# Optimization experiments

Measured on AMD Instinct MI355X. Metric: run time of the kernel, lower is better.

Reference implementation:

```python
import jax, jax.numpy as jnp
import numpy as np

B = 128          # batch of predictions
C = 1024         # number of constraints
N = 512          # number of atoms appearing in constraints (minimal subset)
NUM_CLASSES = 1024
BODY_P = 0.02    # body sparsity


def setup_inputs() -> dict:
    rng = np.random.default_rng(0)
    # distinct sorted atom indices into the full class space
    atoms = np.sort(rng.permutation(NUM_CLASSES)[:N]).astype(np.int64)
    # each constraint has one head literal: one-hot in pos_head OR neg_head
    head_atom = rng.integers(0, N, size=C)
    head_sign = rng.random(C) < 0.5
    pos_head = np.zeros((C, N), np.float32)
    neg_head = np.zeros((C, N), np.float32)
    rows = np.arange(C)
    pos_head[rows[head_sign], head_atom[head_sign]] = 1.0
    neg_head[rows[~head_sign], head_atom[~head_sign]] = 1.0
    # sparse disjoint 0/1 body masks, head atom excluded from its own body
    pos_body = (rng.random((C, N)) < BODY_P).astype(np.float32)
    neg_body = ((rng.random((C, N)) < BODY_P) & (pos_body == 0)).astype(np.float32)
    pos_body[rows, head_atom] = 0.0
    neg_body[rows, head_atom] = 0.0
    key = jax.random.key(0)
    preds = jax.random.uniform(key, (B, NUM_CLASSES), dtype=jnp.float32)  # probs in [0,1]
    return {
        "preds": preds,
        "pos_head": jnp.asarray(pos_head),
        "neg_head": jnp.asarray(neg_head),
        "pos_body": jnp.asarray(pos_body),
        "neg_body": jnp.asarray(neg_body),
        "atoms": jnp.asarray(atoms),
    }


def reference(preds, pos_head, neg_head, pos_body, neg_body, atoms):
    # to_minimal: gather atom subset  [B, N]
    m = preds[:, atoms]
    # body_rev[b,c,j] = pos_body + m*(neg_body - pos_body)
    #   = (1-m) where body literal positive, m where negative, 0 otherwise
    body_rev = pos_body[None] + m[:, None, :] * (neg_body - pos_body)[None]  # [B,C,N]
    # candidate body satisfaction degree per constraint
    body_min = 1.0 - jnp.max(body_rev, axis=2)  # [B,C]
    # scatter candidates to head atoms via one-hot head masks (max-reduce over cons)
    lb = jnp.max(body_min[:, :, None] * pos_head[None], axis=1)        # [B,N]
    ub = 1.0 - jnp.max(body_min[:, :, None] * neg_head[None], axis=1)  # [B,N]
    lo = jnp.minimum(lb, ub)
    hi = jnp.maximum(lb, ub)
    updated = jnp.maximum(lo, jnp.minimum(hi, m))
    # from_minimal: scatter updated atoms back into full prediction vector
    return preds.at[:, atoms].set(updated)
```

## Files before the change

### kernel.cpp

```cpp
#include <hip/hip_runtime.h>

#define Bsz 128
#define Csz 1024
#define Nsz 512
#define NCsz 1024
#define CAP 64

__global__ __launch_bounds__(256) void k_pre(
    const float* __restrict__ preds,
    const float* __restrict__ pos_head, const float* __restrict__ neg_head,
    const float* __restrict__ pos_body, const float* __restrict__ neg_body,
    const int* __restrict__ atoms,
    float* __restrict__ mT, unsigned* __restrict__ bounds,
    int* __restrict__ pos_list, int* __restrict__ neg_list,
    int* __restrict__ pos_cnt, int* __restrict__ neg_cnt,
    int* __restrict__ head_of,
    float* __restrict__ out)
{
    int blk = blockIdx.x, tid = threadIdx.x;
    if (blk < 128) {
        ((uint4*)bounds)[blk * 256 + tid] = make_uint4(0u, 0u, 0u, 0u);
    } else if (blk < 384) {
        int b   = tid & (Bsz - 1);
        int col = 2 * (blk - 128) + (tid >> 7);
        mT[col * Bsz + b] = preds[b * NCsz + atoms[col]];
    } else if (blk < 640) {
        __shared__ int cnts[4][2];
        int wave = tid >> 6, lane = tid & 63;
        int c = (blk - 384) * 4 + wave;
        if (lane == 0) { cnts[wave][0] = 0; cnts[wave][1] = 0; }
        const float4* pb4 = (const float4*)(pos_body + c * Nsz);
        const float4* nb4 = (const float4*)(neg_body + c * Nsz);
        const float4* ph4 = (const float4*)(pos_head + c * Nsz);
        const float4* nh4 = (const float4*)(neg_head + c * Nsz);
        for (int k = 0; k < 2; k++) {
            int q = k * 64 + lane;
            float4 p  = pb4[q];
            float4 nb = nb4[q];
            float4 ph = ph4[q];
            float4 nh = nh4[q];
            int n0 = q * 4;
            if (p.x  != 0.f) { int s = atomicAdd(&cnts[wave][0], 1); if (s < CAP) pos_list[c * CAP + s] = n0;     }
            if (p.y  != 0.f) { int s = atomicAdd(&cnts[wave][0], 1); if (s < CAP) pos_list[c * CAP + s] = n0 + 1; }
            if (p.z  != 0.f) { int s = atomicAdd(&cnts[wave][0], 1); if (s < CAP) pos_list[c * CAP + s] = n0 + 2; }
            if (p.w  != 0.f) { int s = atomicAdd(&cnts[wave][0], 1); if (s < CAP) pos_list[c * CAP + s] = n0 + 3; }
            if (nb.x != 0.f) { int s = atomicAdd(&cnts[wave][1], 1); if (s < CAP) neg_list[c * CAP + s] = n0;     }
            if (nb.y != 0.f) { int s = atomicAdd(&cnts[wave][1], 1); if (s < CAP) neg_list[c * CAP + s] = n0 + 1; }
            if (nb.z != 0.f) { int s = atomicAdd(&cnts[wave][1], 1); if (s < CAP) neg_list[c * CAP + s] = n0 + 2; }
            if (nb.w != 0.f) { int s = atomicAdd(&cnts[wave][1], 1); if (s < CAP) neg_list[c * CAP + s] = n0 + 3; }
            if (ph.x != 0.f) head_of[c] = ((n0    ) << 1) | 1;
            if (ph.y != 0.f) head_of[c] = ((n0 + 1) << 1) | 1;
            if (ph.z != 0.f) head_of[c] = ((n0 + 2) << 1) | 1;
            if (ph.w != 0.f) head_of[c] = ((n0 + 3) << 1) | 1;
            if (nh.x != 0.f) head_of[c] = ((n0    ) << 1);
            if (nh.y != 0.f) head_of[c] = ((n0 + 1) << 1);
            if (nh.z != 0.f) head_of[c] = ((n0 + 2) << 1);
            if (nh.w != 0.f) head_of[c] = ((n0 + 3) << 1);
        }
        if (lane == 0) {
            pos_cnt[c] = min(cnts[wave][0], CAP);
            neg_cnt[c] = min(cnts[wave][1], CAP);
        }
    } else {
        int q = (blk - 640) * 256 + tid;
        ((float4*)out)[q] = ((const float4*)preds)[q];
    }
}

__global__ __launch_bounds__(256) void k_body(
    const float* __restrict__ mT,
    const int* __restrict__ pos_list, const int* __restrict__ neg_list,
    const int* __restrict__ pos_cnt, const int* __restrict__ neg_cnt,
    const int* __restrict__ head_of,
    unsigned* __restrict__ bounds)
{
    __shared__ int sp[2][CAP];
    __shared__ int sn[2][CAP];
    int tid = threadIdx.x;
    int cl = tid >> 7, r = tid & 127;
    int c = blockIdx.x * 2 + cl;
    if (r < CAP) sp[cl][r]       = pos_list[c * CAP + r];
    else         sn[cl][r - CAP] = neg_list[c * CAP + (r - CAP)];
    __syncthreads();

    int b  = tid & (Bsz - 1);
    int pc = pos_cnt[c], nc = neg_cnt[c];
    float acc = 0.f;
    #pragma unroll 4
    for (int e = 0; e < pc; e++) acc = fmaxf(acc, 1.f - mT[sp[cl][e] * Bsz + b]);
    #pragma unroll 4
    for (int e = 0; e < nc; e++) acc = fmaxf(acc, mT[sn[cl][e] * Bsz + b]);

    int h = head_of[c];
    unsigned* lbmax = bounds;
    unsigned* ubmax = bounds + Bsz * Nsz;
    unsigned* dst = (h & 1) ? lbmax : ubmax;
    atomicMax(dst + (h >> 1) * Bsz + b, __float_as_uint(1.f - acc));
}

__global__ __launch_bounds__(256) void k_final(
    const float* __restrict__ mT,
    const unsigned* __restrict__ bounds,
    const int* __restrict__ atoms, float* __restrict__ out)
{
    int t = blockIdx.x * 256 + threadIdx.x;
    int b = t & (Bsz - 1), n = t >> 7;
    int i = n * Bsz + b;
    float m  = mT[i];
    float lb = __uint_as_float(bounds[i]);
    float ub = 1.f - __uint_as_float(bounds[Bsz * Nsz + i]);
    float lo = fminf(lb, ub), hi = fmaxf(lb, ub);
    out[b * NCsz + atoms[n]] = fmaxf(lo, fminf(hi, m));
}

extern "C" void kernel_launch(void* const* d_in, const int* in_sizes, int n_in,
                              void* d_out, int out_size, void* d_ws, size_t ws_size,
                              hipStream_t stream)
{
    const float* preds    = (const float*)d_in[0];
    const float* pos_head = (const float*)d_in[1];
    const float* neg_head = (const float*)d_in[2];
    const float* pos_body = (const float*)d_in[3];
    const float* neg_body = (const float*)d_in[4];
    const int*   atoms    = (const int*)d_in[5];
    float* out = (float*)d_out;

    char* ws = (char*)d_ws;
    float*    mT       = (float*)(ws);
    unsigned* bounds   = (unsigned*)(ws + 65536u * 4);
    int*      pos_list = (int*)(ws + 196608u * 4);
    int*      neg_list = (int*)(ws + 262144u * 4);
    int*      pos_cnt  = (int*)(ws + 327680u * 4);
    int*      neg_cnt  = pos_cnt + Csz;
    int*      head_of  = neg_cnt + Csz;

    k_pre<<<768, 256, 0, stream>>>(preds, pos_head, neg_head, pos_body, neg_body, atoms,
                                   mT, bounds, pos_list, neg_list,
                                   pos_cnt, neg_cnt, head_of, out);

    k_body<<<Csz / 2, 256, 0, stream>>>(mT, pos_list, neg_list, pos_cnt, neg_cnt,
                                        head_of, bounds);

    k_final<<<256, 256, 0, stream>>>(mT, bounds, atoms, out);
}
```

Baseline: 77.12 us.

## Fuse body, bound and scatter stages into one per-batch LDS kernel

Replaces the three-kernel pipeline with a constraint scan kernel plus a single per-batch-row kernel. That kernel gathers the atom row into shared memory, evaluates all constraints from a merged, transposed literal list, reduces the bounds with shared-memory atomics and writes the full output row through an inverse atom map. This removes the global bounds zeroing, the global atomics, the mT transpose buffer, the separate copy of preds to out, and one launch. In exchange only 128 blocks run, and every block re-reads the literal lists.

```diff
diff --git a/kernel.cpp b/kernel.cpp
--- a/kernel.cpp
+++ b/kernel.cpp
@@ -4,113 +4,101 @@
 #define Csz 1024
 #define Nsz 512
 #define NCsz 1024
-#define CAP 64
+#define CAPT 96
 
-__global__ __launch_bounds__(256) void k_pre(
-    const float* __restrict__ preds,
+__global__ __launch_bounds__(256) void k_scan(
     const float* __restrict__ pos_head, const float* __restrict__ neg_head,
     const float* __restrict__ pos_body, const float* __restrict__ neg_body,
+    int* __restrict__ litT, int* __restrict__ lit_cnt, int* __restrict__ head_of)
+{
+    __shared__ int cnts[4];
+    int tid = threadIdx.x;
+    int wave = tid >> 6, lane = tid & 63;
+    int c = blockIdx.x * 4 + wave;
+    if (lane == 0) cnts[wave] = 0;
+    const float4* pb4 = (const float4*)(pos_body + c * Nsz);
+    const float4* nb4 = (const float4*)(neg_body + c * Nsz);
+    const float4* ph4 = (const float4*)(pos_head + c * Nsz);
+    const float4* nh4 = (const float4*)(neg_head + c * Nsz);
+    for (int k = 0; k < 2; k++) {
+        int q = k * 64 + lane;
+        float4 p  = pb4[q];
+        float4 nb = nb4[q];
+        float4 ph = ph4[q];
+        float4 nh = nh4[q];
+        int n0 = q * 4;
+        if (p.x  != 0.f) { int s = atomicAdd(&cnts[wave], 1); if (s < CAPT) litT[s * Csz + c] = (n0    ) << 1; }
+        if (p.y  != 0.f) { int s = atomicAdd(&cnts[wave], 1); if (s < CAPT) litT[s * Csz + c] = (n0 + 1) << 1; }
+        if (p.z  != 0.f) { int s = atomicAdd(&cnts[wave], 1); if (s < CAPT) litT[s * Csz + c] = (n0 + 2) << 1; }
+        if (p.w  != 0.f) { int s = atomicAdd(&cnts[wave], 1); if (s < CAPT) litT[s * Csz + c] = (n0 + 3) << 1; }
+        if (nb.x != 0.f) { int s = atomicAdd(&cnts[wave], 1); if (s < CAPT) litT[s * Csz + c] = ((n0    ) << 1) | 1; }
+        if (nb.y != 0.f) { int s = atomicAdd(&cnts[wave], 1); if (s < CAPT) litT[s * Csz + c] = ((n0 + 1) << 1) | 1; }
+        if (nb.z != 0.f) { int s = atomicAdd(&cnts[wave], 1); if (s < CAPT) litT[s * Csz + c] = ((n0 + 2) << 1) | 1; }
+        if (nb.w != 0.f) { int s = atomicAdd(&cnts[wave], 1); if (s < CAPT) litT[s * Csz + c] = ((n0 + 3) << 1) | 1; }
+        if (ph.x != 0.f) head_of[c] = ((n0    ) << 1) | 1;
+        if (ph.y != 0.f) head_of[c] = ((n0 + 1) << 1) | 1;
+        if (ph.z != 0.f) head_of[c] = ((n0 + 2) << 1) | 1;
+        if (ph.w != 0.f) head_of[c] = ((n0 + 3) << 1) | 1;
+        if (nh.x != 0.f) head_of[c] = ((n0    ) << 1);
+        if (nh.y != 0.f) head_of[c] = ((n0 + 1) << 1);
+        if (nh.z != 0.f) head_of[c] = ((n0 + 2) << 1);
+        if (nh.w != 0.f) head_of[c] = ((n0 + 3) << 1);
+    }
+    if (lane == 0) lit_cnt[c] = min(cnts[wave], CAPT);
+}
+
+__global__ __launch_bounds__(1024) void k_apply(
+    const float* __restrict__ preds,
     const int* __restrict__ atoms,
-    float* __restrict__ mT, unsigned* __restrict__ bounds,
-    int* __restrict__ pos_list, int* __restrict__ neg_list,
-    int* __restrict__ pos_cnt, int* __restrict__ neg_cnt,
-    int* __restrict__ head_of,
+    const int* __restrict__ litT, const int* __restrict__ lit_cnt,
+    const int* __restrict__ head_of,
     float* __restrict__ out)
 {
-    int blk = blockIdx.x, tid = threadIdx.x;
-    if (blk < 128) {
-        ((uint4*)bounds)[blk * 256 + tid] = make_uint4(0u, 0u, 0u, 0u);
-    } else if (blk < 384) {
-        int b   = tid & (Bsz - 1);
-        int col = 2 * (blk - 128) + (tid >> 7);
-        mT[col * Bsz + b] = preds[b * NCsz + atoms[col]];
-    } else if (blk < 640) {
-        __shared__ int cnts[4][2];
-        int wave = tid >> 6, lane = tid & 63;
-        int c = (blk - 384) * 4 + wave;
-        if (lane == 0) { cnts[wave][0] = 0; cnts[wave][1] = 0; }
-        const float4* pb4 = (const float4*)(pos_body + c * Nsz);
-        const float4* nb4 = (const float4*)(neg_body + c * Nsz);
-        const float4* ph4 = (const float4*)(pos_head + c * Nsz);
-        const float4* nh4 = (const float4*)(neg_head + c * Nsz);
-        for (int k = 0; k < 2; k++) {
-            int q = k * 64 + lane;
-            float4 p  = pb4[q];
-            float4 nb = nb4[q];
-            float4 ph = ph4[q];
-            float4 nh = nh4[q];
-            int n0 = q * 4;
-            if (p.x  != 0.f) { int s = atomicAdd(&cnts[wave][0], 1); if (s < CAP) pos_list[c * CAP + s] = n0;     }
-            if (p.y  != 0.f) { int s = atomicAdd(&cnts[wave][0], 1); if (s < CAP) pos_list[c * CAP + s] = n0 + 1; }
-            if (p.z  != 0.f) { int s = atomicAdd(&cnts[wave][0], 1); if (s < CAP) pos_list[c * CAP + s] = n0 + 2; }
-            if (p.w  != 0.f) { int s = atomicAdd(&cnts[wave][0], 1); if (s < CAP) pos_list[c * CAP + s] = n0 + 3; }
-            if (nb.x != 0.f) { int s = atomicAdd(&cnts[wave][1], 1); if (s < CAP) neg_list[c * CAP + s] = n0;     }
-            if (nb.y != 0.f) { int s = atomicAdd(&cnts[wave][1], 1); if (s < CAP) neg_list[c * CAP + s] = n0 + 1; }
-            if (nb.z != 0.f) { int s = atomicAdd(&cnts[wave][1], 1); if (s < CAP) neg_list[c * CAP + s] = n0 + 2; }
-            if (nb.w != 0.f) { int s = atomicAdd(&cnts[wave][1], 1); if (s < CAP) neg_list[c * CAP + s] = n0 + 3; }
-            if (ph.x != 0.f) head_of[c] = ((n0    ) << 1) | 1;
-            if (ph.y != 0.f) head_of[c] = ((n0 + 1) << 1) | 1;
-            if (ph.z != 0.f) head_of[c] = ((n0 + 2) << 1) | 1;
-            if (ph.w != 0.f) head_of[c] = ((n0 + 3) << 1) | 1;
-            if (nh.x != 0.f) head_of[c] = ((n0    ) << 1);
-            if (nh.y != 0.f) head_of[c] = ((n0 + 1) << 1);
-            if (nh.z != 0.f) head_of[c] = ((n0 + 2) << 1);
-            if (nh.w != 0.f) head_of[c] = ((n0 + 3) << 1);
-        }
-        if (lane == 0) {
-            pos_cnt[c] = min(cnts[wave][0], CAP);
-            neg_cnt[c] = min(cnts[wave][1], CAP);
-        }
-    } else {
-        int q = (blk - 640) * 256 + tid;
-        ((float4*)out)[q] = ((const float4*)preds)[q];
+    __shared__ float    m[Nsz];
+    __shared__ unsigned lbq[Nsz];
+    __shared__ unsigned ubq[Nsz];
+    __shared__ short    inv[NCsz];
+
+    const int b = blockIdx.x, tid = threadIdx.x;
+
+    inv[tid] = -1;
+    if (tid < Nsz) { lbq[tid] = 0u; ubq[tid] = 0u; }
+    __syncthreads();
+    if (tid < Nsz) {
+        int a = atoms[tid];
+        m[tid] = preds[b * NCsz + a];
+        inv[a] = (short)tid;
     }
-}
-
-__global__ __launch_bounds__(256) void k_body(
-    const float* __restrict__ mT,
-    const int* __restrict__ pos_list, const int* __restrict__ neg_list,
-    const int* __restrict__ pos_cnt, const int* __restrict__ neg_cnt,
-    const int* __restrict__ head_of,
-    unsigned* __restrict__ bounds)
-{
-    __shared__ int sp[2][CAP];
-    __shared__ int sn[2][CAP];
-    int tid = threadIdx.x;
-    int cl = tid >> 7, r = tid & 127;
-    int c = blockIdx.x * 2 + cl;
-    if (r < CAP) sp[cl][r]       = pos_list[c * CAP + r];
-    else         sn[cl][r - CAP] = neg_list[c * CAP + (r - CAP)];
     __syncthreads();
 
-    int b  = tid & (Bsz - 1);
-    int pc = pos_cnt[c], nc = neg_cnt[c];
-    float acc = 0.f;
-    #pragma unroll 4
-    for (int e = 0; e < pc; e++) acc = fmaxf(acc, 1.f - mT[sp[cl][e] * Bsz + b]);
-    #pragma unroll 4
-    for (int e = 0; e < nc; e++) acc = fmaxf(acc, mT[sn[cl][e] * Bsz + b]);
+    {
+        int c = tid;
+        int cnt = lit_cnt[c];
+        float acc = 0.f;
+        #pragma unroll 4
+        for (int e = 0; e < cnt; e++) {
+            int v = litT[e * Csz + c];
+            float x = m[v >> 1];
+            acc = fmaxf(acc, (v & 1) ? x : 1.f - x);
+        }
+        float bm = 1.f - acc;
+        int h = head_of[c];
+        unsigned* dst = (h & 1) ? lbq : ubq;
+        atomicMax(&dst[h >> 1], __float_as_uint(bm));
+    }
+    __syncthreads();
 
-    int h = head_of[c];
-    unsigned* lbmax = bounds;
-    unsigned* ubmax = bounds + Bsz * Nsz;
-    unsigned* dst = (h & 1) ? lbmax : ubmax;
-    atomicMax(dst + (h >> 1) * Bsz + b, __float_as_uint(1.f - acc));
-}
-
-__global__ __launch_bounds__(256) void k_final(
-    const float* __restrict__ mT,
-    const unsigned* __restrict__ bounds,
-    const int* __restrict__ atoms, float* __restrict__ out)
-{
-    int t = blockIdx.x * 256 + threadIdx.x;
-    int b = t & (Bsz - 1), n = t >> 7;
-    int i = n * Bsz + b;
-    float m  = mT[i];
-    float lb = __uint_as_float(bounds[i]);
-    float ub = 1.f - __uint_as_float(bounds[Bsz * Nsz + i]);
-    float lo = fminf(lb, ub), hi = fmaxf(lb, ub);
-    out[b * NCsz + atoms[n]] = fmaxf(lo, fminf(hi, m));
+    {
+        float v = preds[b * NCsz + tid];
+        int n = inv[tid];
+        if (n >= 0) {
+            float lb = __uint_as_float(lbq[n]);
+            float ub = 1.f - __uint_as_float(ubq[n]);
+            float lo = fminf(lb, ub), hi = fmaxf(lb, ub);
+            v = fmaxf(lo, fminf(hi, v));
+        }
+        out[b * NCsz + tid] = v;
+    }
 }
 
 extern "C" void kernel_launch(void* const* d_in, const int* in_sizes, int n_in,
@@ -126,20 +114,12 @@
     float* out = (float*)d_out;
 
     char* ws = (char*)d_ws;
-    float*    mT       = (float*)(ws);
-    unsigned* bounds   = (unsigned*)(ws + 65536u * 4);
-    int*      pos_list = (int*)(ws + 196608u * 4);
-    int*      neg_list = (int*)(ws + 262144u * 4);
-    int*      pos_cnt  = (int*)(ws + 327680u * 4);
-    int*      neg_cnt  = pos_cnt + Csz;
-    int*      head_of  = neg_cnt + Csz;
+    int* litT    = (int*)(ws);
+    int* lit_cnt = (int*)(ws + (size_t)CAPT * Csz * 4);
+    int* head_of = lit_cnt + Csz;
 
-    k_pre<<<768, 256, 0, stream>>>(preds, pos_head, neg_head, pos_body, neg_body, atoms,
-                                   mT, bounds, pos_list, neg_list,
-                                   pos_cnt, neg_cnt, head_of, out);
+    k_scan<<<256, 256, 0, stream>>>(pos_head, neg_head, pos_body, neg_body,
+                                    litT, lit_cnt, head_of);
 
-    k_body<<<Csz / 2, 256, 0, stream>>>(mT, pos_list, neg_list, pos_cnt, neg_cnt,
-                                        head_of, bounds);
-
-    k_final<<<256, 256, 0, stream>>>(mT, bounds, atoms, out);
+    k_apply<<<Bsz, 1024, 0, stream>>>(preds, atoms, litT, lit_cnt, head_of, out);
 }
```

New measurement: 77.68 us. No clear change (+0.7%).
